# Kernel optimization log

Hardware: AMD Instinct MI355X
Metric: run time of the kernel (lower is better)

## Reference

```python
import jax, jax.numpy as jnp
import numpy as np
from jax import lax

# ---- static config (ProposalLayer config object) ----
BASE_SIZE = 16
RATIOS = np.array([0.5, 1.0, 2.0])
SCALES = np.array([8.0, 16.0, 32.0])
STRIDE = 16
PRE_NMS_TOPN = 6000
POST_NMS_TOPN = 300
MIN_THRESHOLD = 16.0
NMS_THRESH = 0.7
IMG_W = 4096
IMG_H = 2048
NEG_INF = jnp.float32(-1e30)


def _generate_anchors(base_size, ratios, scales):
    w = h = float(base_size)
    x_ctr = y_ctr = 0.5 * (base_size - 1)
    size = w * h
    size_ratios = size / ratios
    ws = np.round(np.sqrt(size_ratios))          # (R,)
    hs = np.round(ws * ratios)                   # (R,)
    ws = (ws[:, None] * scales[None, :]).ravel() # (R*S,)
    hs = (hs[:, None] * scales[None, :]).ravel()
    anchors = np.stack([x_ctr - 0.5 * (ws - 1), y_ctr - 0.5 * (hs - 1),
                        x_ctr + 0.5 * (ws - 1), y_ctr + 0.5 * (hs - 1)], axis=1)
    return anchors.astype(np.float32)            # (A, 4) in x1,y1,x2,y2


def _all_anchors(height, width, stride):
    anchors = _generate_anchors(BASE_SIZE, RATIOS, SCALES)      # (A,4)
    sx = np.arange(width) * stride
    sy = np.arange(height) * stride
    mx, my = np.meshgrid(sx, sy)                                # (H,W) each
    shifts = np.stack([mx.ravel(), my.ravel(), mx.ravel(), my.ravel()], axis=1)
    shifts = shifts.reshape(-1, 1, 4).astype(np.float32)        # (K,1,4), K iterates h-major
    return (anchors[None] + shifts).reshape(-1, 4)              # (K*A, 4)


def _decode(deltas, anchors):
    # deltas: (B, N, 4); anchors: (N, 4) -> boxes (B, N, 4)
    aw = anchors[:, 2] - anchors[:, 0] + 1.0
    ah = anchors[:, 3] - anchors[:, 1] + 1.0
    acx = anchors[:, 0] + 0.5 * (aw - 1.0)
    acy = anchors[:, 1] + 0.5 * (ah - 1.0)
    dx, dy, dw, dh = deltas[..., 0], deltas[..., 1], deltas[..., 2], deltas[..., 3]
    pcx = dx * aw + acx
    pcy = dy * ah + acy
    pw = jnp.exp(dw) * aw
    ph = jnp.exp(dh) * ah
    return jnp.stack([pcx - 0.5 * pw, pcy - 0.5 * ph,
                      pcx + 0.5 * pw, pcy + 0.5 * ph], axis=-1)


def _nms_single(boxes, scores):
    # boxes (N,4), scores (N,) -> greedy NMS, fixed POST_NMS_TOPN outputs
    areas = (boxes[:, 2] - boxes[:, 0] + 1.0) * (boxes[:, 3] - boxes[:, 1] + 1.0)

    def body(live, _):
        i = jnp.argmax(live)
        box = boxes[i]
        sc = scores[i]
        xx1 = jnp.maximum(box[0], boxes[:, 0])
        yy1 = jnp.maximum(box[1], boxes[:, 1])
        xx2 = jnp.minimum(box[2], boxes[:, 2])
        yy2 = jnp.minimum(box[3], boxes[:, 3])
        inter = jnp.maximum(xx2 - xx1 + 1.0, 0.0) * jnp.maximum(yy2 - yy1 + 1.0, 0.0)
        iou = inter / (areas[i] + areas - inter)
        live = jnp.where(iou > NMS_THRESH, NEG_INF, live)
        live = live.at[i].set(NEG_INF)
        return live, (box, sc)

    _, (out_boxes, out_scores) = lax.scan(body, scores, None, length=POST_NMS_TOPN)
    return out_boxes, out_scores  # (P,4), (P,)


def reference(labels_pred, bbox_reg):
    B = labels_pred.shape[0]
    H, W = labels_pred.shape[-2:]
    anchors = jnp.asarray(_all_anchors(H, W, STRIDE))           # (K*A,4)

    # objectness score = fg channel after (B,2A,H,W)->(B,H,W,2A)->(B,KA,2)
    scores = jnp.transpose(labels_pred, (0, 2, 3, 1)).reshape(B, -1, 2)[..., 1]
    deltas = jnp.transpose(bbox_reg, (0, 2, 3, 1)).reshape(B, -1, 4)

    boxes = _decode(deltas, anchors)                            # (B,KA,4)
    x = jnp.clip(boxes[..., 0::2], 0.0, IMG_W - 1.0)
    y = jnp.clip(boxes[..., 1::2], 0.0, IMG_H - 1.0)
    boxes = jnp.stack([x[..., 0], y[..., 0], x[..., 1], y[..., 1]], axis=-1)

    keep = ((boxes[..., 2] - boxes[..., 0] + 1.0 >= MIN_THRESHOLD) &
            (boxes[..., 3] - boxes[..., 1] + 1.0 >= MIN_THRESHOLD))
    masked = jnp.where(keep, scores, NEG_INF)

    # pre-NMS top-k of kept anchors by score (assumes keep.sum >= PRE_NMS_TOPN)
    top_scores_masked, idx = lax.top_k(masked, PRE_NMS_TOPN)    # (B,P)
    top_scores = jnp.take_along_axis(scores, idx, axis=1)
    top_boxes = jnp.take_along_axis(boxes, idx[..., None], axis=1)

    out_boxes, out_scores = jax.vmap(_nms_single)(top_boxes, top_scores)
    return out_boxes, out_scores


def setup_inputs() -> dict:
    key = jax.random.key(0)
    k1, k2 = jax.random.split(key)
    labels_pred = jax.random.normal(k1, (16, 18, 128, 256), dtype=jnp.float32)
    bbox_reg = jax.random.normal(k2, (16, 36, 128, 256), dtype=jnp.float32)
    return {"labels_pred": labels_pred, "bbox_reg": bbox_reg}
```

## Files before the change

kernel.cpp:

```cpp
#include <hip/hip_runtime.h>
#include <stdint.h>

#define NBATCH 16
#define NANCH  9
#define NHGT   128
#define NWID   256
#define NHW    (NHGT * NWID)
#define NTOT   (NHW * NANCH)
#define PRE    6000
#define POST   300
#define CAPN   8192
#define BINS   8192
#define BIN_SHIFT 19
#define NWORDS 94
#define NWSTRIDE 96
#define RROWS  384
#define NGROUPS (RROWS / 8)
#define JQ     1536

#define MIDP 0x1.6666668p-1

__device__ __constant__ float c_AW[NANCH] = {184.f,368.f,736.f,128.f,256.f,512.f,88.f,176.f,352.f};
__device__ __constant__ float c_AH[NANCH] = {96.f,192.f,384.f,128.f,256.f,512.f,176.f,352.f,704.f};

__device__ __forceinline__ uint32_t f2key(float f) {
    uint32_t u = __float_as_uint(f);
    return (u & 0x80000000u) ? ~u : (u | 0x80000000u);
}

__device__ __forceinline__ bool iou_sup(const float4 bi, float areaI, const float4 bj, float areaJ) {
    float xx1 = fmaxf(bi.x, bj.x);
    float yy1 = fmaxf(bi.y, bj.y);
    float xx2 = fminf(bi.z, bj.z);
    float yy2 = fminf(bi.w, bj.w);
    float iw = fmaxf(__fadd_rn(__fsub_rn(xx2, xx1), 1.f), 0.f);
    float ih = fmaxf(__fadd_rn(__fsub_rn(yy2, yy1), 1.f), 0.f);
    float inter = __fmul_rn(iw, ih);
    float uni = __fsub_rn(__fadd_rn(areaI, areaJ), inter);
    return ((double)inter >= (double)uni * MIDP);
}

__device__ __forceinline__ bool decode_clip(float dx, float dy, float dw, float dh,
                                            float aw, float ah, float acx, float acy,
                                            float& x1, float& y1, float& x2, float& y2) {
    float pcx = __fadd_rn(__fmul_rn(dx, aw), acx);
    float pcy = __fadd_rn(__fmul_rn(dy, ah), acy);
    float pw  = __fmul_rn(expf(dw), aw);
    float ph  = __fmul_rn(expf(dh), ah);
    float hx  = __fmul_rn(0.5f, pw);
    float hy  = __fmul_rn(0.5f, ph);
    x1 = __fsub_rn(pcx, hx);
    y1 = __fsub_rn(pcy, hy);
    x2 = __fadd_rn(pcx, hx);
    y2 = __fadd_rn(pcy, hy);
    x1 = fminf(fmaxf(x1, 0.f), 4095.f);
    x2 = fminf(fmaxf(x2, 0.f), 4095.f);
    y1 = fminf(fmaxf(y1, 0.f), 2047.f);
    y2 = fminf(fmaxf(y2, 0.f), 2047.f);
    float wpl = __fadd_rn(__fsub_rn(x2, x1), 1.f);
    float hpl = __fadd_rn(__fsub_rn(y2, y1), 1.f);
    return (wpl >= 16.f) && (hpl >= 16.f);
}

__global__ __launch_bounds__(256) void k_zero(uint4* __restrict__ ghist4,
                                              uint32_t* __restrict__ cntthr) {
    int g = blockIdx.x * 256 + threadIdx.x;
    if (blockIdx.x < 128) {
        ghist4[g] = make_uint4(0, 0, 0, 0);
    } else {
        if (threadIdx.x < 32) cntthr[threadIdx.x] = 0;
    }
}

__global__ __launch_bounds__(256) void k_hist(const float* __restrict__ lab,
                                              const float* __restrict__ reg,
                                              uint32_t* __restrict__ ghist,
                                              uint32_t* __restrict__ keys) {
    __shared__ uint32_t hist[BINS];
    for (int i = threadIdx.x; i < BINS; i += 256) hist[i] = 0;
    __syncthreads();
    int b = blockIdx.x >> 5, sub = blockIdx.x & 31;
    int hw = (sub << 10) | (threadIdx.x << 2);
    int h = hw >> 8, w = hw & 255;
    const float* lb = lab + (size_t)b * 18 * NHW + hw;
    const float* rb = reg + (size_t)b * 36 * NHW + hw;
    uint32_t* kb = keys + (size_t)b * NANCH * NHW + hw;
    float acy  = (float)(h * 16) + 7.5f;
    float acx0 = (float)(w * 16) + 7.5f;
    float acx1 = acx0 + 16.0f;
    float acx2 = acx0 + 32.0f;
    float acx3 = acx0 + 48.0f;
#pragma unroll
    for (int a = 0; a < NANCH; ++a) {
        float4 s  = *(const float4*)&lb[(2 * a + 1) * NHW];
        float4 dx = *(const float4*)&rb[(4 * a + 0) * NHW];
        float4 dy = *(const float4*)&rb[(4 * a + 1) * NHW];
        float4 dwv = *(const float4*)&rb[(4 * a + 2) * NHW];
        float4 dhv = *(const float4*)&rb[(4 * a + 3) * NHW];
        float x1, y1, x2, y2;
        bool k0 = decode_clip(dx.x, dy.x, dwv.x, dhv.x, c_AW[a], c_AH[a], acx0, acy, x1, y1, x2, y2);
        bool k1 = decode_clip(dx.y, dy.y, dwv.y, dhv.y, c_AW[a], c_AH[a], acx1, acy, x1, y1, x2, y2);
        bool k2 = decode_clip(dx.z, dy.z, dwv.z, dhv.z, c_AW[a], c_AH[a], acx2, acy, x1, y1, x2, y2);
        bool k3 = decode_clip(dx.w, dy.w, dwv.w, dhv.w, c_AW[a], c_AH[a], acx3, acy, x1, y1, x2, y2);
        uint32_t key0 = f2key(k0 ? s.x : -1e30f);
        uint32_t key1 = f2key(k1 ? s.y : -1e30f);
        uint32_t key2 = f2key(k2 ? s.z : -1e30f);
        uint32_t key3 = f2key(k3 ? s.w : -1e30f);
        *(uint4*)&kb[a * NHW] = make_uint4(key0, key1, key2, key3);
        atomicAdd(&hist[key0 >> BIN_SHIFT], 1u);
        atomicAdd(&hist[key1 >> BIN_SHIFT], 1u);
        atomicAdd(&hist[key2 >> BIN_SHIFT], 1u);
        atomicAdd(&hist[key3 >> BIN_SHIFT], 1u);
    }
    __syncthreads();
    uint32_t* gh = ghist + ((size_t)b << 13);
    for (int i = threadIdx.x; i < BINS; i += 256) {
        uint32_t c = hist[i];
        if (c) atomicAdd(&gh[i], c);
    }
}

__global__ __launch_bounds__(256) void k_thresh(const uint32_t* __restrict__ ghist,
                                                uint32_t* __restrict__ thresh) {
    __shared__ uint32_t part[256];
    int b = blockIdx.x;
    const uint32_t* gh = ghist + ((size_t)b << 13);
    uint32_t p = 0;
    int base = threadIdx.x * 32;
    for (int k = 0; k < 32; ++k) p += gh[base + k];
    part[threadIdx.x] = p;
    __syncthreads();
    if (threadIdx.x == 0) {
        uint32_t cum = 0;
        int tb = 0;
        for (int c = 255; c >= 0; --c) {
            if (cum + part[c] >= (uint32_t)PRE) {
                for (int i = 31; i >= 0; --i) {
                    cum += gh[c * 32 + i];
                    if (cum >= (uint32_t)PRE) { tb = c * 32 + i; break; }
                }
                break;
            }
            cum += part[c];
        }
        thresh[b] = (uint32_t)tb << BIN_SHIFT;
    }
}

__global__ __launch_bounds__(256) void k_compact(const uint32_t* __restrict__ keys,
                                                 const uint32_t* __restrict__ thresh,
                                                 uint32_t* __restrict__ cnt,
                                                 uint64_t* __restrict__ cand) {
    __shared__ uint64_t stage[2304];
    __shared__ uint32_t sCount;
    __shared__ uint32_t sBase;
    if (threadIdx.x == 0) sCount = 0;
    __syncthreads();
    int bid = blockIdx.x;
    int b = bid >> 7;
    int hw = ((bid & 127) << 8) | threadIdx.x;
    int lane = threadIdx.x & 63;
    const uint32_t* kb = keys + (size_t)b * NANCH * NHW + hw;
    uint32_t th = thresh[b];
#pragma unroll
    for (int a = 0; a < NANCH; ++a) {
        uint32_t key = kb[a * NHW];
        bool valid = (key >= th);
        uint64_t mask = __ballot(valid);
        if (mask) {
            int leader = __ffsll((unsigned long long)mask) - 1;
            uint32_t wb = 0;
            if (lane == leader) wb = atomicAdd(&sCount, (uint32_t)__popcll(mask));
            wb = (uint32_t)__shfl((int)wb, leader);
            if (valid) {
                int rank = __popcll(mask & ((1ull << lane) - 1ull));
                uint32_t n = (uint32_t)(hw * NANCH + a);
                stage[wb + rank] = ((uint64_t)key << 32) | (uint32_t)(~n);
            }
        }
    }
    __syncthreads();
    if (threadIdx.x == 0) sBase = atomicAdd(&cnt[b], sCount);
    __syncthreads();
    uint32_t total = sCount, base = sBase;
    for (uint32_t i = threadIdx.x; i < total; i += 256) {
        uint32_t pos = base + i;
        if (pos < (uint32_t)CAPN) cand[(size_t)b * CAPN + pos] = stage[i];
    }
}

__global__ __launch_bounds__(512) void k_sortA(const uint32_t* __restrict__ cnt,
                                               uint64_t* __restrict__ cand) {
    __shared__ uint64_t sm[1024];
    int b = blockIdx.x >> 3, c = blockIdx.x & 7;
    uint32_t C = cnt[b];
    if (C > (uint32_t)CAPN) C = CAPN;
    uint64_t* cb = cand + (size_t)b * CAPN;
    int base = c << 10;
    for (int li = threadIdx.x; li < 1024; li += 512) {
        int gi = base + li;
        sm[li] = (gi < (int)C) ? cb[gi] : 0ull;
    }
    __syncthreads();
    for (int k = 2; k <= 1024; k <<= 1) {
        for (int j = k >> 1; j > 0; j >>= 1) {
            for (int li = threadIdx.x; li < 1024; li += 512) {
                int lxj = li ^ j;
                if (lxj > li) {
                    uint64_t va = sm[li], vb = sm[lxj];
                    bool up = ((li & k) == 0);
                    bool sw = up ? (va < vb) : (va > vb);
                    if (sw) { sm[li] = vb; sm[lxj] = va; }
                }
            }
            __syncthreads();
        }
    }
    for (int li = threadIdx.x; li < 1024; li += 512) cb[base + li] = sm[li];
}

__global__ __launch_bounds__(256) void k_merge(const uint64_t* __restrict__ src,
                                               uint64_t* __restrict__ dst,
                                               int Rlog) {
    int g = blockIdx.x * 256 + threadIdx.x;
    if (g >= NBATCH * CAPN) return;
    int b = g >> 13;
    int p = g & (CAPN - 1);
    int R = 1 << Rlog;
    int pair = p >> (Rlog + 1);
    int q = p & ((R << 1) - 1);
    const uint64_t* A = src + (size_t)b * CAPN + ((size_t)(pair << 1) << Rlog);
    const uint64_t* B = A + R;
    int lo = (q > R) ? (q - R) : 0;
    int hi = (q < R) ? q : R;
    while (lo < hi) {
        int mid = (lo + hi) >> 1;
        if (A[mid] > B[q - mid - 1]) lo = mid + 1; else hi = mid;
    }
    int i = lo, j = q - lo;
    uint64_t aV = (i < R) ? A[i] : 0ull;
    uint64_t bV = (j < R) ? B[j] : 0ull;
    dst[(size_t)b * CAPN + p] = (aV > bV) ? aV : bV;
}

__global__ __launch_bounds__(256) void k_mergegather(const uint64_t* __restrict__ cand,
                                                     const float* __restrict__ lab,
                                                     const float* __restrict__ reg,
                                                     float4* __restrict__ boxes,
                                                     float* __restrict__ scores) {
    int g = blockIdx.x * 256 + threadIdx.x;
    if (g >= NBATCH * PRE) return;
    int b = g / PRE, p = g - b * PRE;
    const uint64_t* A = cand + (size_t)b * CAPN;
    const uint64_t* B = A + 4096;
    int lo = (p > 4096) ? (p - 4096) : 0;
    int hi = (p < 4096) ? p : 4096;
    while (lo < hi) {
        int mid = (lo + hi) >> 1;
        if (A[mid] > B[p - mid - 1]) lo = mid + 1; else hi = mid;
    }
    int i = lo, j = p - lo;
    uint64_t aV = (i < 4096) ? A[i] : 0ull;
    uint64_t bV = (j < 4096) ? B[j] : 0ull;
    uint64_t v = (aV > bV) ? aV : bV;
    uint32_t n = ~(uint32_t)(v & 0xFFFFFFFFull);
    if (n >= (uint32_t)NTOT) n = 0;
    int a = (int)(n % NANCH);
    int hw = (int)(n / NANCH);
    int w = hw & 255, h = hw >> 8;
    const float* lb0 = lab + (size_t)b * 18 * NHW;
    const float* rb0 = reg + (size_t)b * 36 * NHW;
    float s  = lb0[(2 * a + 1) * NHW + hw];
    float dx = rb0[(4 * a + 0) * NHW + hw];
    float dy = rb0[(4 * a + 1) * NHW + hw];
    float dwv = rb0[(4 * a + 2) * NHW + hw];
    float dhv = rb0[(4 * a + 3) * NHW + hw];
    float acx = (float)(w * 16) + 7.5f;
    float acy = (float)(h * 16) + 7.5f;
    float x1, y1, x2, y2;
    decode_clip(dx, dy, dwv, dhv, c_AW[a], c_AH[a], acx, acy, x1, y1, x2, y2);
    boxes[b * PRE + p] = make_float4(x1, y1, x2, y2);
    scores[b * PRE + p] = s;
}

__global__ __launch_bounds__(512) void k_iou(const float4* __restrict__ boxes,
                                             uint64_t* __restrict__ supp) {
    __shared__ float4 lb[JQ];
    __shared__ float  la[JQ];
    int quad = blockIdx.x & 3;
    int rblk = (blockIdx.x >> 2) & 15;
    int b    = blockIdx.x >> 6;
    const float4* bb = boxes + b * PRE;
    int jbase  = quad * JQ;
    int jcount = (quad == 3) ? (PRE - 3 * JQ) : JQ;
    for (int i = threadIdx.x; i < jcount; i += 512) {
        float4 v = bb[jbase + i];
        lb[i] = v;
        la[i] = __fmul_rn(__fadd_rn(__fsub_rn(v.z, v.x), 1.f),
                          __fadd_rn(__fsub_rn(v.w, v.y), 1.f));
    }
    __syncthreads();
    int wave = threadIdx.x >> 6, lane = threadIdx.x & 63;
    int wlo = quad * 24;
    int whi = (quad == 3) ? NWORDS : (wlo + 24);
    int r0 = rblk + 16 * wave;
    int r1 = r0 + 128;
    int r2 = r0 + 256;
    float4 bi0 = bb[r0];
    float4 bi1 = bb[r1];
    float4 bi2 = bb[r2];
    float a0 = __fmul_rn(__fadd_rn(__fsub_rn(bi0.z, bi0.x), 1.f),
                         __fadd_rn(__fsub_rn(bi0.w, bi0.y), 1.f));
    float a1 = __fmul_rn(__fadd_rn(__fsub_rn(bi1.z, bi1.x), 1.f),
                         __fadd_rn(__fsub_rn(bi1.w, bi1.y), 1.f));
    float a2 = __fmul_rn(__fadd_rn(__fsub_rn(bi2.z, bi2.x), 1.f),
                         __fadd_rn(__fsub_rn(bi2.w, bi2.y), 1.f));
    uint64_t keep0 = 0ull, keep1 = 0ull, keep2 = 0ull;
    int w0 = r0 >> 6;
    int wstart = (wlo > w0) ? wlo : w0;
    for (int w = wstart; w < whi; ++w) {
        int j = (w << 6) | lane;
        bool s0 = false, s1 = false, s2 = false;
        if (j < PRE) {
            int idx = j - jbase;
            float4 bj = lb[idx];
            float aj = la[idx];
            s0 = iou_sup(bi0, a0, bj, aj);
            s1 = iou_sup(bi1, a1, bj, aj);
            s2 = iou_sup(bi2, a2, bj, aj);
        }
        uint64_t m0 = __ballot(s0);
        uint64_t m1 = __ballot(s1);
        uint64_t m2 = __ballot(s2);
        if (lane == w - wlo) { keep0 = m0; keep1 = m1; keep2 = m2; }
    }
    uint64_t* sr0 = supp + ((size_t)b * RROWS + r0) * NWSTRIDE;
    uint64_t* sr1 = supp + ((size_t)b * RROWS + r1) * NWSTRIDE;
    uint64_t* sr2 = supp + ((size_t)b * RROWS + r2) * NWSTRIDE;
    if (lane < 24) {
        uint64_t k0 = keep0, k1 = keep1, k2 = keep2;
        if (quad == 3 && lane >= 22) { k0 = 0; k1 = 0; k2 = 0; }
        sr0[wlo + lane] = k0;
        sr1[wlo + lane] = k1;
        sr2[wlo + lane] = k2;
    }
}

#define ISSUE(BUF, GRP) do {                                                               \
    int _g = (GRP); if (_g > NGROUPS - 1) _g = NGROUPS - 1;                                \
    int _jb = _g << 3;                                                                     \
    const ulonglong2* _p = (const ulonglong2*)(sbase + (size_t)_jb * NWSTRIDE) + lclamp;   \
    BUF##0 = _p[0];   BUF##1 = _p[48];  BUF##2 = _p[96];  BUF##3 = _p[144];                \
    BUF##4 = _p[192]; BUF##5 = _p[240]; BUF##6 = _p[288]; BUF##7 = _p[336];                \
    __builtin_amdgcn_sched_barrier(0);          \
} while (0)

#define ROWP(RD, JB, R) {                                                                  \
    if (((curw >> (((JB) & 63) + (R))) & 1ull) != 0ull) {                                  \
        if (lane == 0) idxb[t] = (uint32_t)((JB) + (R));                                   \
        v0 &= ~RD.x; v1 &= ~RD.y;                                                          \
        int _w = ((JB) + (R)) >> 6;                                                        \
        uint64_t _sw = (uint64_t)__shfl((long long)((_w & 1) ? RD.y : RD.x), _w >> 1);     \
        curw &= ~_sw;                                                                      \
        ++t;                                                                               \
        if (t >= POST) goto walk_done;                                                     \
    }                                                                                      \
}

#define PROC(BUF, GRP) do {                                                                \
    int _jb2 = (GRP) << 3;                                                                 \
    if ((_jb2 & 63) == 0) {                                                                \
        int _wi = _jb2 >> 6;                                                               \
        uint64_t _c0 = (uint64_t)__shfl((long long)v0, _wi >> 1);                          \
        uint64_t _c1 = (uint64_t)__shfl((long long)v1, _wi >> 1);                          \
        curw = (_wi & 1) ? _c1 : _c0;                                                      \
    }                                                                                      \
    ROWP(BUF##0, _jb2, 0); ROWP(BUF##1, _jb2, 1); ROWP(BUF##2, _jb2, 2); ROWP(BUF##3, _jb2, 3); \
    ROWP(BUF##4, _jb2, 4); ROWP(BUF##5, _jb2, 5); ROWP(BUF##6, _jb2, 6); ROWP(BUF##7, _jb2, 7); \
} while (0)

__global__ __launch_bounds__(64, 1) void k_walk(const uint64_t* __restrict__ supp,
                                                uint32_t* __restrict__ flags,
                                                uint32_t* __restrict__ tsave,
                                                uint64_t* __restrict__ aliveSv,
                                                uint32_t* __restrict__ idxAll) {
    int b = blockIdx.x;
    int lane = threadIdx.x;
    int lclamp = (lane < 48) ? lane : 47;
    uint32_t* idxb = idxAll + b * POST;
    const uint64_t* sbase = supp + (size_t)b * RROWS * NWSTRIDE;
    uint64_t v0, v1;
    if (lane < 46)       { v0 = ~0ull; v1 = ~0ull; }
    else if (lane == 46) { v0 = ~0ull; v1 = (1ull << 48) - 1ull; }
    else                 { v0 = 0ull;  v1 = 0ull; }
    uint64_t curw = 0;
    int t = 0;
    int flag = 0;
    ulonglong2 A0,A1,A2,A3,A4,A5,A6,A7;
    ulonglong2 B0,B1,B2,B3,B4,B5,B6,B7;
    ulonglong2 C0,C1,C2,C3,C4,C5,C6,C7;
    ulonglong2 D0,D1,D2,D3,D4,D5,D6,D7;
    ulonglong2 E0,E1,E2,E3,E4,E5,E6,E7;
    ulonglong2 F0,F1,F2,F3,F4,F5,F6,F7;
    ISSUE(A, 0); ISSUE(B, 1); ISSUE(C, 2); ISSUE(D, 3); ISSUE(E, 4); ISSUE(F, 5);
    for (int g = 0; g < NGROUPS; g += 6) {
        PROC(A, g);     ISSUE(A, g + 6);
        PROC(B, g + 1); ISSUE(B, g + 7);
        PROC(C, g + 2); ISSUE(C, g + 8);
        PROC(D, g + 3); ISSUE(D, g + 9);
        PROC(E, g + 4); ISSUE(E, g + 10);
        PROC(F, g + 5); ISSUE(F, g + 11);
    }
    {
        unsigned long long anyAlive = __ballot((v0 | v1) != 0ull);
        if (anyAlive == 0ull) {
            if (lane == 0) for (int tt = t; tt < POST; ++tt) idxb[tt] = 0u;
        } else {
            if (2 * lane < NWORDS)     aliveSv[b * NWORDS + 2 * lane] = v0;
            if (2 * lane + 1 < NWORDS) aliveSv[b * NWORDS + 2 * lane + 1] = v1;
            if (lane == 0) tsave[b] = (uint32_t)t;
            flag = 1;
        }
    }
walk_done:
    if (lane == 0) flags[b] = (uint32_t)flag;
}

__global__ __launch_bounds__(512) void k_resume(const float4* __restrict__ boxes,
                                                const uint32_t* __restrict__ flags,
                                                const uint32_t* __restrict__ tsave,
                                                const uint64_t* __restrict__ aliveSv,
                                                uint32_t* __restrict__ idxAll) {
    int b = blockIdx.x;
    if (flags[b] == 0) return;
    __shared__ uint64_t alive[NWORDS];
    __shared__ uint32_t sCur;
    int tid = threadIdx.x;
    const float4* bb = boxes + b * PRE;
    uint32_t* idxb = idxAll + b * POST;
    if (tid < NWORDS) alive[tid] = aliveSv[b * NWORDS + tid];
    __syncthreads();
    int t0 = (int)tsave[b];
    for (int t = t0; t < POST; ++t) {
        if (tid == 0) sCur = 0xFFFFFFFFu;
        __syncthreads();
        if (tid < NWORDS) {
            uint64_t wd = alive[tid];
            if (wd) atomicMin(&sCur, (uint32_t)(tid * 64 + (__ffsll((unsigned long long)wd) - 1)));
        }
        __syncthreads();
        uint32_t cur = sCur;
        uint32_t e = (cur < (uint32_t)PRE) ? cur : 0u;
        if (tid == 0) {
            idxb[t] = e;
            if (cur < (uint32_t)PRE)
                atomicAnd(&alive[cur >> 6], ~(1ull << (cur & 63)));
        }
        if (cur < (uint32_t)PRE) {
            float4 bc = bb[e];
            float areaC = __fmul_rn(__fadd_rn(__fsub_rn(bc.z, bc.x), 1.f),
                                    __fadd_rn(__fsub_rn(bc.w, bc.y), 1.f));
            for (uint32_t j = cur + 1 + tid; j < (uint32_t)PRE; j += 512) {
                uint64_t wd = alive[j >> 6];
                if ((wd >> (j & 63)) & 1ull) {
                    float4 bj = bb[j];
                    float areaJ = __fmul_rn(__fadd_rn(__fsub_rn(bj.z, bj.x), 1.f),
                                            __fadd_rn(__fsub_rn(bj.w, bj.y), 1.f));
                    if (iou_sup(bc, areaC, bj, areaJ))
                        atomicAnd(&alive[j >> 6], ~(1ull << (j & 63)));
                }
            }
        }
        __syncthreads();
    }
}

__global__ __launch_bounds__(256) void k_out(const float4* __restrict__ boxes,
                                             const float* __restrict__ scores,
                                             const uint32_t* __restrict__ idxAll,
                                             float* __restrict__ out) {
    int g = blockIdx.x * 256 + threadIdx.x;
    if (g >= NBATCH * POST) return;
    int b = g / POST;
    uint32_t i = idxAll[g];
    if (i >= (uint32_t)PRE) i = 0;
    float4 bc = boxes[b * PRE + i];
    size_t ob = (size_t)g * 4;
    out[ob + 0] = bc.x; out[ob + 1] = bc.y;
    out[ob + 2] = bc.z; out[ob + 3] = bc.w;
    out[(size_t)NBATCH * POST * 4 + g] = scores[b * PRE + i];
}

extern "C" void kernel_launch(void* const* d_in, const int* in_sizes, int n_in,
                              void* d_out, int out_size, void* d_ws, size_t ws_size,
                              hipStream_t stream) {
    (void)in_sizes; (void)n_in; (void)out_size; (void)ws_size;
    const float* lab = (const float*)d_in[0];
    const float* reg = (const float*)d_in[1];
    float* out = (float*)d_out;
    char* ws = (char*)d_ws;

    uint32_t* ghist  = (uint32_t*)(ws + 0);
    uint32_t* cnt    = (uint32_t*)(ws + 524288);
    uint32_t* thr    = (uint32_t*)(ws + 524352);
    uint64_t* cand   = (uint64_t*)(ws + 524416);
    float4*   boxes  = (float4*)  (ws + 1572992);
    float*    scores = (float*)   (ws + 3108992);
    uint64_t* supp   = (uint64_t*)(ws + 3492992);
    uint32_t* flags  = (uint32_t*)(ws + 8211584);
    uint32_t* tsave  = (uint32_t*)(ws + 8211648);
    uint64_t* aliveS = (uint64_t*)(ws + 8211712);
    uint32_t* idx    = (uint32_t*)(ws + 8223744);
    uint32_t* keys   = (uint32_t*)(ws + 8242944);
    uint64_t* cand2  = (uint64_t*)(ws + 27117312);

    k_zero       <<<129, 256, 0, stream>>>((uint4*)ghist, cnt);
    k_hist       <<<512, 256, 0, stream>>>(lab, reg, ghist, keys);
    k_thresh     <<<NBATCH, 256, 0, stream>>>(ghist, thr);
    k_compact    <<<2048, 256, 0, stream>>>(keys, thr, cnt, cand);
    k_sortA      <<<NBATCH * 8, 512, 0, stream>>>(cnt, cand);
    k_merge      <<<NBATCH * CAPN / 256, 256, 0, stream>>>(cand, cand2, 10);
    k_merge      <<<NBATCH * CAPN / 256, 256, 0, stream>>>(cand2, cand, 11);
    k_mergegather<<<(NBATCH * PRE + 255) / 256, 256, 0, stream>>>(cand, lab, reg, boxes, scores);
    k_iou        <<<NBATCH * 64, 512, 0, stream>>>(boxes, supp);
    k_walk       <<<NBATCH, 64, 0, stream>>>(supp, flags, tsave, aliveS, idx);
    k_resume     <<<NBATCH, 512, 0, stream>>>(boxes, flags, tsave, aliveS, idx);
    k_out        <<<(NBATCH * POST + 255) / 256, 256, 0, stream>>>(boxes, scores, idx, out);
}
```

Before: 182.8 us.

## Track only first 384 alive bits in walk; rebuild full alive mask in resume

The single-wave NMS walk now keeps just the 6 alive words covering the 384 precomputed rows, replicated in every lane. Each row is one 64-bit load per lane and is applied with wave shuffles, instead of two 64-bit words per lane covering all 6000 boxes. The walk no longer saves the full alive mask. The resume kernel rebuilds it by replaying the accepted indices against the suppression matrix. This shrinks the walk's load traffic and register use but adds 6 shuffles per accepted box and a serial replay loop in resume. The walk also no longer takes the early-exit path when no boxes remain alive.

```diff
diff --git a/kernel.cpp b/kernel.cpp
--- a/kernel.cpp
+++ b/kernel.cpp
@@ -346,62 +346,52 @@
     }
 }
 
+#define GETW(W3) ((W3) == 0 ? s0 : (W3) == 1 ? s1 : (W3) == 2 ? s2 : \
+                  (W3) == 3 ? s3 : (W3) == 4 ? s4 : s5)
+
 #define ISSUE(BUF, GRP) do {                                                               \
     int _g = (GRP); if (_g > NGROUPS - 1) _g = NGROUPS - 1;                                \
-    int _jb = _g << 3;                                                                     \
-    const ulonglong2* _p = (const ulonglong2*)(sbase + (size_t)_jb * NWSTRIDE) + lclamp;   \
-    BUF##0 = _p[0];   BUF##1 = _p[48];  BUF##2 = _p[96];  BUF##3 = _p[144];                \
-    BUF##4 = _p[192]; BUF##5 = _p[240]; BUF##6 = _p[288]; BUF##7 = _p[336];                \
-    __builtin_amdgcn_sched_barrier(0);          \
+    BUF = sbase[(size_t)(_g << 3) * NWSTRIDE + laneoff];                                   \
+    __builtin_amdgcn_sched_barrier(0);                                                     \
 } while (0)
 
-#define ROWP(RD, JB, R) {                                                                  \
+#define ROWP(BUF, JB, R) {                                                                 \
     if (((curw >> (((JB) & 63) + (R))) & 1ull) != 0ull) {                                  \
         if (lane == 0) idxb[t] = (uint32_t)((JB) + (R));                                   \
-        v0 &= ~RD.x; v1 &= ~RD.y;                                                          \
-        int _w = ((JB) + (R)) >> 6;                                                        \
-        uint64_t _sw = (uint64_t)__shfl((long long)((_w & 1) ? RD.y : RD.x), _w >> 1);     \
-        curw &= ~_sw;                                                                      \
+        s0 &= ~(uint64_t)__shfl((long long)BUF, (R) * 6 + 0);                              \
+        s1 &= ~(uint64_t)__shfl((long long)BUF, (R) * 6 + 1);                              \
+        s2 &= ~(uint64_t)__shfl((long long)BUF, (R) * 6 + 2);                              \
+        s3 &= ~(uint64_t)__shfl((long long)BUF, (R) * 6 + 3);                              \
+        s4 &= ~(uint64_t)__shfl((long long)BUF, (R) * 6 + 4);                              \
+        s5 &= ~(uint64_t)__shfl((long long)BUF, (R) * 6 + 5);                              \
+        curw = GETW(_w3);                                                                  \
         ++t;                                                                               \
         if (t >= POST) goto walk_done;                                                     \
     }                                                                                      \
 }
 
 #define PROC(BUF, GRP) do {                                                                \
-    int _jb2 = (GRP) << 3;                                                                 \
-    if ((_jb2 & 63) == 0) {                                                                \
-        int _wi = _jb2 >> 6;                                                               \
-        uint64_t _c0 = (uint64_t)__shfl((long long)v0, _wi >> 1);                          \
-        uint64_t _c1 = (uint64_t)__shfl((long long)v1, _wi >> 1);                          \
-        curw = (_wi & 1) ? _c1 : _c0;                                                      \
-    }                                                                                      \
-    ROWP(BUF##0, _jb2, 0); ROWP(BUF##1, _jb2, 1); ROWP(BUF##2, _jb2, 2); ROWP(BUF##3, _jb2, 3); \
-    ROWP(BUF##4, _jb2, 4); ROWP(BUF##5, _jb2, 5); ROWP(BUF##6, _jb2, 6); ROWP(BUF##7, _jb2, 7); \
+    int _jb = (GRP) << 3;                                                                  \
+    int _w3 = _jb >> 6;                                                                    \
+    uint64_t curw = GETW(_w3);                                                             \
+    ROWP(BUF, _jb, 0); ROWP(BUF, _jb, 1); ROWP(BUF, _jb, 2); ROWP(BUF, _jb, 3);            \
+    ROWP(BUF, _jb, 4); ROWP(BUF, _jb, 5); ROWP(BUF, _jb, 6); ROWP(BUF, _jb, 7);            \
 } while (0)
 
 __global__ __launch_bounds__(64, 1) void k_walk(const uint64_t* __restrict__ supp,
                                                 uint32_t* __restrict__ flags,
                                                 uint32_t* __restrict__ tsave,
-                                                uint64_t* __restrict__ aliveSv,
                                                 uint32_t* __restrict__ idxAll) {
     int b = blockIdx.x;
     int lane = threadIdx.x;
-    int lclamp = (lane < 48) ? lane : 47;
+    int lcl = (lane < 48) ? lane : 47;
+    int laneoff = (lcl / 6) * NWSTRIDE + (lcl % 6);
     uint32_t* idxb = idxAll + b * POST;
     const uint64_t* sbase = supp + (size_t)b * RROWS * NWSTRIDE;
-    uint64_t v0, v1;
-    if (lane < 46)       { v0 = ~0ull; v1 = ~0ull; }
-    else if (lane == 46) { v0 = ~0ull; v1 = (1ull << 48) - 1ull; }
-    else                 { v0 = 0ull;  v1 = 0ull; }
-    uint64_t curw = 0;
+    uint64_t s0 = ~0ull, s1 = ~0ull, s2 = ~0ull, s3 = ~0ull, s4 = ~0ull, s5 = ~0ull;
     int t = 0;
     int flag = 0;
-    ulonglong2 A0,A1,A2,A3,A4,A5,A6,A7;
-    ulonglong2 B0,B1,B2,B3,B4,B5,B6,B7;
-    ulonglong2 C0,C1,C2,C3,C4,C5,C6,C7;
-    ulonglong2 D0,D1,D2,D3,D4,D5,D6,D7;
-    ulonglong2 E0,E1,E2,E3,E4,E5,E6,E7;
-    ulonglong2 F0,F1,F2,F3,F4,F5,F6,F7;
+    uint64_t A, B, C, D, E, F;
     ISSUE(A, 0); ISSUE(B, 1); ISSUE(C, 2); ISSUE(D, 3); ISSUE(E, 4); ISSUE(F, 5);
     for (int g = 0; g < NGROUPS; g += 6) {
         PROC(A, g);     ISSUE(A, g + 6);
@@ -411,25 +401,16 @@
         PROC(E, g + 4); ISSUE(E, g + 10);
         PROC(F, g + 5); ISSUE(F, g + 11);
     }
-    {
-        unsigned long long anyAlive = __ballot((v0 | v1) != 0ull);
-        if (anyAlive == 0ull) {
-            if (lane == 0) for (int tt = t; tt < POST; ++tt) idxb[tt] = 0u;
-        } else {
-            if (2 * lane < NWORDS)     aliveSv[b * NWORDS + 2 * lane] = v0;
-            if (2 * lane + 1 < NWORDS) aliveSv[b * NWORDS + 2 * lane + 1] = v1;
-            if (lane == 0) tsave[b] = (uint32_t)t;
-            flag = 1;
-        }
-    }
+    if (lane == 0) tsave[b] = (uint32_t)t;
+    flag = 1;
 walk_done:
     if (lane == 0) flags[b] = (uint32_t)flag;
 }
 
 __global__ __launch_bounds__(512) void k_resume(const float4* __restrict__ boxes,
+                                                const uint64_t* __restrict__ supp,
                                                 const uint32_t* __restrict__ flags,
                                                 const uint32_t* __restrict__ tsave,
-                                                const uint64_t* __restrict__ aliveSv,
                                                 uint32_t* __restrict__ idxAll) {
     int b = blockIdx.x;
     if (flags[b] == 0) return;
@@ -438,9 +419,15 @@
     int tid = threadIdx.x;
     const float4* bb = boxes + b * PRE;
     uint32_t* idxb = idxAll + b * POST;
-    if (tid < NWORDS) alive[tid] = aliveSv[b * NWORDS + tid];
+    if (tid < NWORDS) alive[tid] = (tid == NWORDS - 1) ? ((1ull << 48) - 1ull) : ~0ull;
     __syncthreads();
     int t0 = (int)tsave[b];
+    for (int tt = 0; tt < t0; ++tt) {
+        uint32_t r = idxb[tt];
+        if (tid < NWORDS)
+            alive[tid] &= ~supp[((size_t)b * RROWS + r) * NWSTRIDE + tid];
+    }
+    __syncthreads();
     for (int t = t0; t < POST; ++t) {
         if (tid == 0) sCur = 0xFFFFFFFFu;
         __syncthreads();
@@ -509,10 +496,9 @@
     uint64_t* supp   = (uint64_t*)(ws + 3492992);
     uint32_t* flags  = (uint32_t*)(ws + 8211584);
     uint32_t* tsave  = (uint32_t*)(ws + 8211648);
-    uint64_t* aliveS = (uint64_t*)(ws + 8211712);
-    uint32_t* idx    = (uint32_t*)(ws + 8223744);
-    uint32_t* keys   = (uint32_t*)(ws + 8242944);
-    uint64_t* cand2  = (uint64_t*)(ws + 27117312);
+    uint32_t* idx    = (uint32_t*)(ws + 8211712);
+    uint32_t* keys   = (uint32_t*)(ws + 8230912);
+    uint64_t* cand2  = (uint64_t*)(ws + 27105280);
 
     k_zero       <<<129, 256, 0, stream>>>((uint4*)ghist, cnt);
     k_hist       <<<512, 256, 0, stream>>>(lab, reg, ghist, keys);
@@ -523,7 +509,7 @@
     k_merge      <<<NBATCH * CAPN / 256, 256, 0, stream>>>(cand2, cand, 11);
     k_mergegather<<<(NBATCH * PRE + 255) / 256, 256, 0, stream>>>(cand, lab, reg, boxes, scores);
     k_iou        <<<NBATCH * 64, 512, 0, stream>>>(boxes, supp);
-    k_walk       <<<NBATCH, 64, 0, stream>>>(supp, flags, tsave, aliveS, idx);
-    k_resume     <<<NBATCH, 512, 0, stream>>>(boxes, flags, tsave, aliveS, idx);
+    k_walk       <<<NBATCH, 64, 0, stream>>>(supp, flags, tsave, idx);
+    k_resume     <<<NBATCH, 512, 0, stream>>>(boxes, supp, flags, tsave, idx);
     k_out        <<<(NBATCH * POST + 255) / 256, 256, 0, stream>>>(boxes, scores, idx, out);
 }
```

New measurement: 222.0 us. 21.4% more time.
